# Kernel tuning notes

Measured on AMD Instinct MI355X. Metric: run time of the kernel, lower is better.

Reference implementation:

```python
import jax, jax.numpy as jnp
import numpy as np

NUM_HEADS = 8
OUT_FEATURES = 64
ALPHA = 0.2


def setup_inputs() -> dict:
    key = jax.random.key(0)
    k1, k2, k3, k4 = jax.random.split(key, 4)
    B, N, E, F_IN = 2, 8192, 4096, 256
    x = jax.random.normal(k1, (B, N, F_IN), dtype=jnp.float32)
    H = jax.random.uniform(k2, (N, E), dtype=jnp.float32)
    # xavier-like scaled params
    W = jax.random.normal(k3, (F_IN, OUT_FEATURES * NUM_HEADS), dtype=jnp.float32) * 0.05
    a_vertices = jax.random.normal(k4, (OUT_FEATURES, 1), dtype=jnp.float32) * 0.1
    return {"x": x, "H": H, "W": W, "a_vertices": a_vertices}


def reference(x, H, W, a_vertices):
    B, N, _ = x.shape
    # Wh: (B, N, heads, out)
    Wh = jnp.matmul(x, W).reshape(B, N, NUM_HEADS, OUT_FEATURES)
    # per-node, per-head attention logit: (B, N, heads)
    av = jax.nn.leaky_relu(jnp.einsum('bnhd,d->bnh', Wh, a_vertices[:, 0]), ALPHA)
    # edge attention: softmax over edges (torch dim=0 of (E, heads))
    ae = jax.nn.softmax(jnp.einsum('ne,bnh->beh', H, av), axis=1)  # (B, E, heads)
    # aggregate node features onto edges: (B, E, heads, out)
    m = jnp.einsum('ne,bnhd->behd', H, Wh)
    # scatter back to nodes with edge-attention weighting: (B, N, heads, out)
    out = jnp.einsum('ne,beh,behd->bnhd', H, ae, m)
    return out.reshape(B, N, NUM_HEADS * OUT_FEATURES)
```

## Files before the change

kernel.cpp:

```cpp
#include <hip/hip_runtime.h>

#define N_NODES 8192
#define N_EDGES 4096
#define F_INS   256
#define HEADS   8
#define DOUT    64
#define HDIM    512
#define CCOMB   1024
#define BATCH   2

typedef __bf16 bf16x8 __attribute__((ext_vector_type(8)));
typedef __bf16 bf16x4 __attribute__((ext_vector_type(4)));
typedef float  f32x4  __attribute__((ext_vector_type(4)));

__device__ __forceinline__ void gld_lds16(const __bf16* g, __bf16* l) {
    __builtin_amdgcn_global_load_lds(
        (const __attribute__((address_space(1))) void*)g,
        (__attribute__((address_space(3))) void*)l, 16, 0, 0);
}

__launch_bounds__(256)
__global__ void convert_H_logits_kernel(const float* __restrict__ H,
                                        const float* __restrict__ av,
                                        __bf16* __restrict__ Hb,
                                        __bf16* __restrict__ HbT,
                                        float* __restrict__ logits) {
    __shared__ float lav[512 * 16];
    __shared__ __bf16 tile[32][33];
    __shared__ float red[256 * 16];
    int t = threadIdx.x;
    int e0 = blockIdx.x * 32;
    int n0 = blockIdx.y * 512;
    for (int p = t; p < 8192; p += 256) {
        int b = p >> 12, rem = p & 4095, i = rem >> 3, h = rem & 7;
        lav[i * 16 + b * 8 + h] = av[(size_t)b * (N_NODES * 8) + (size_t)(n0 + i) * 8 + h];
    }
    __syncthreads();
    int c = t & 31, r0 = t >> 5;
    float acc[16];
#pragma unroll
    for (int q = 0; q < 16; ++q) acc[q] = 0.f;
    for (int sub = 0; sub < 16; ++sub) {
        int nb = n0 + sub * 32;
#pragma unroll
        for (int p = 0; p < 4; ++p) {
            int r = p * 8 + r0;
            float v = H[(size_t)(nb + r) * N_EDGES + e0 + c];
            __bf16 bv = (__bf16)v;
            Hb[(size_t)(nb + r) * N_EDGES + e0 + c] = bv;
            tile[r][c] = bv;
            const float* lr = &lav[(sub * 32 + r) * 16];
#pragma unroll
            for (int q = 0; q < 16; ++q) acc[q] += v * lr[q];
        }
        __syncthreads();
#pragma unroll
        for (int p = 0; p < 4; ++p) {
            int er = p * 8 + r0;
            HbT[(size_t)(e0 + er) * N_NODES + nb + c] = tile[c][er];
        }
        __syncthreads();
    }
#pragma unroll
    for (int q = 0; q < 16; ++q) red[t * 16 + q] = acc[q];
    __syncthreads();
    for (int o = t; o < 512; o += 256) {
        int e = o & 31, q = o >> 5;
        float s = 0.f;
#pragma unroll
        for (int r8 = 0; r8 < 8; ++r8) s += red[(r8 * 32 + e) * 16 + q];
        atomicAdd(&logits[(size_t)q * N_EDGES + e0 + e], s);
    }
}

__launch_bounds__(256)
__global__ void wbt_kernel(const float* __restrict__ W, __bf16* __restrict__ WbT) {
    int i = blockIdx.x * 256 + threadIdx.x;
    int c = i >> 8, f = i & 255;
    WbT[i] = (__bf16)W[(size_t)f * HDIM + c];
}

__launch_bounds__(256)
__global__ void wa_kernel(const float* __restrict__ W, const float* __restrict__ a,
                          float* __restrict__ Wa) {
    int i = blockIdx.x * 256 + threadIdx.x;
    if (i >= F_INS * HEADS) return;
    int f = i >> 3, h = i & 7;
    float s = 0.f;
#pragma unroll 8
    for (int d = 0; d < DOUT; ++d) s += W[(size_t)f * HDIM + h * DOUT + d] * a[d];
    Wa[i] = s;
}

__launch_bounds__(256)
__global__ void av_kernel(const float* __restrict__ x, const float* __restrict__ Wa,
                          float* __restrict__ av, __bf16* __restrict__ xb) {
    __shared__ float lx[32][257];
    __shared__ float lwa[F_INS * HEADS];
    int t = threadIdx.x;
    size_t row0 = (size_t)blockIdx.x * 32;
    for (int p = t; p < F_INS * HEADS; p += 256) lwa[p] = Wa[p];
#pragma unroll
    for (int p = 0; p < 32; ++p) {
        float v = x[(row0 + p) * F_INS + t];
        lx[p][t] = v;
        xb[(row0 + p) * F_INS + t] = (__bf16)v;
    }
    __syncthreads();
    int r = t >> 3, h = t & 7;
    float acc = 0.f;
#pragma unroll 8
    for (int f = 0; f < F_INS; ++f) acc += lx[r][f] * lwa[f * 8 + h];
    av[(row0 + r) * 8 + h] = acc > 0.f ? acc : 0.2f * acc;
}

__launch_bounds__(256)
__global__ void softmax_kernel(float* __restrict__ logits) {
    __shared__ float red[4];
    __shared__ float reds[4];
    int t = threadIdx.x;
    float* row = logits + (size_t)blockIdx.x * N_EDGES;
    float mx = -1e30f;
    for (int i = t; i < N_EDGES; i += 256) mx = fmaxf(mx, row[i]);
#pragma unroll
    for (int o = 32; o > 0; o >>= 1) mx = fmaxf(mx, __shfl_xor(mx, o, 64));
    if ((t & 63) == 0) red[t >> 6] = mx;
    __syncthreads();
    mx = fmaxf(fmaxf(red[0], red[1]), fmaxf(red[2], red[3]));
    float s = 0.f;
    for (int i = t; i < N_EDGES; i += 256) {
        float v = expf(row[i] - mx);
        row[i] = v;
        s += v;
    }
#pragma unroll
    for (int o = 32; o > 0; o >>= 1) s += __shfl_xor(s, o, 64);
    if ((t & 63) == 0) reds[t >> 6] = s;
    __syncthreads();
    float inv = 1.0f / (reds[0] + reds[1] + reds[2] + reds[3]);
    for (int i = t; i < N_EDGES; i += 256) row[i] *= inv;
}

template <int MODE>
__launch_bounds__(256, 3)
__global__ void gemm_bt(const __bf16* __restrict__ A, const __bf16* __restrict__ BT,
                        int lda, int ldbt, int K,
                        size_t a_bz, size_t bt_bz, size_t out_z,
                        __bf16* __restrict__ outB, int ldo,
                        float* __restrict__ outF) {
    __shared__ __bf16 AsF[8192];
    __shared__ __bf16 BsF[8192];
    int t = threadIdx.x;

    int bx, by, bz;
    if (MODE == 0) {
        bx = blockIdx.x; by = blockIdx.y; bz = blockIdx.z;
    } else if (MODE == 1) {
        int bid = blockIdx.x;
        int xcd = bid & 7, local = bid >> 3;
        bz = local >> 5;
        int rem = local & 31;
        bx = xcd * 4 + (rem >> 3);
        by = rem & 7;
    } else {
        int bid = blockIdx.x;
        bx = bid & 7; by = bid >> 3; bz = 0;
    }

    A  += (size_t)bz * a_bz;
    BT += (size_t)bz * bt_bz;
    if (MODE == 0) outB += (size_t)bz * out_z;
    if (MODE == 1) outF += (size_t)bz * out_z;
    size_t m0 = (size_t)by * 128;
    size_t n0 = (size_t)bx * 128;

    int lane = t & 63, wv = t >> 6;
    int ln = lane & 15, lk = lane >> 4;

    const __bf16* pA[4]; const __bf16* pB[4];
    __bf16* lA[4]; __bf16* lB[4];
#pragma unroll
    for (int p = 0; p < 4; ++p) {
        int bid = wv * 4 + p;
        int mb = bid >> 1, kb = bid & 1;
        pA[p] = A + (m0 + mb * 16 + ln) * (size_t)lda + kb * 32 + lk * 8;
        pB[p] = BT + (n0 + mb * 16 + ln) * (size_t)ldbt + kb * 32 + lk * 8;
        lA[p] = &AsF[bid * 512];
        lB[p] = &BsF[bid * 512];
    }

    int wm16 = (wv & 1) * 4, wn16 = (wv >> 1) * 4;
    f32x4 acc[4][4] = {};

    for (int k0 = 0; k0 < K; k0 += 64) {
        __syncthreads();
#pragma unroll
        for (int p = 0; p < 4; ++p) gld_lds16(pA[p] + k0, lA[p]);
#pragma unroll
        for (int p = 0; p < 4; ++p) gld_lds16(pB[p] + k0, lB[p]);
        __syncthreads();
        bf16x8 af[2][4], bfr[2][4];
#pragma unroll
        for (int ksb = 0; ksb < 2; ++ksb) {
#pragma unroll
            for (int i = 0; i < 4; ++i)
                af[ksb][i] = *(const bf16x8*)&AsF[((wm16 + i) * 2 + ksb) * 512 + lane * 8];
#pragma unroll
            for (int j = 0; j < 4; ++j)
                bfr[ksb][j] = *(const bf16x8*)&BsF[((wn16 + j) * 2 + ksb) * 512 + lane * 8];
        }
#pragma unroll
        for (int ksb = 0; ksb < 2; ++ksb)
#pragma unroll
            for (int i = 0; i < 4; ++i)
#pragma unroll
                for (int j = 0; j < 4; ++j)
                    acc[i][j] = __builtin_amdgcn_mfma_f32_16x16x32_bf16(
                        af[ksb][i], bfr[ksb][j], acc[i][j], 0, 0, 0);
    }

    int wm = (wv & 1) * 64, wn = (wv >> 1) * 64;
#pragma unroll
    for (int i = 0; i < 4; ++i)
#pragma unroll
        for (int j = 0; j < 4; ++j)
#pragma unroll
            for (int rg = 0; rg < 4; ++rg) {
                int gm = (int)m0 + wm + i * 16 + lk * 4 + rg;
                int gc = (int)n0 + wn + j * 16 + ln;
                float v = acc[i][j][rg];
                if (MODE == 0) {
                    outB[(size_t)gm * ldo + gc] = (__bf16)v;
                } else if (MODE == 1) {
                    outF[(size_t)gm * ldo + gc] = v;
                } else {
                    outF[(size_t)(gc >> 9) * ((size_t)N_NODES * HDIM) +
                         (size_t)gm * HDIM + (gc & 511)] = v;
                }
            }
}

__launch_bounds__(256)
__global__ void scale1_kernel(const float* __restrict__ acc1, const float* __restrict__ ae,
                              __bf16* __restrict__ mwT) {
    int i = blockIdx.x * 256 + threadIdx.x;
    size_t base = (size_t)i * 4;
    int c = (int)(base >> 12);
    int e = (int)(base & 4095);
    const size_t slab = (size_t)CCOMB * N_EDGES / 4;
    float4 s0 = ((const float4*)acc1)[i];
    float4 s1 = ((const float4*)acc1)[i + slab];
    float4 s2 = ((const float4*)acc1)[i + 2 * slab];
    float4 s3 = ((const float4*)acc1)[i + 3 * slab];
    float4 a4 = *(const float4*)(ae + ((size_t)(c >> 6) << 12) + e);
    bf16x4 o;
    o.x = (__bf16)((s0.x + s1.x + s2.x + s3.x) * a4.x);
    o.y = (__bf16)((s0.y + s1.y + s2.y + s3.y) * a4.y);
    o.z = (__bf16)((s0.z + s1.z + s2.z + s3.z) * a4.z);
    o.w = (__bf16)((s0.w + s1.w + s2.w + s3.w) * a4.w);
    ((bf16x4*)mwT)[i] = o;
}

extern "C" void kernel_launch(void* const* d_in, const int* in_sizes, int n_in,
                              void* d_out, int out_size, void* d_ws, size_t ws_size,
                              hipStream_t stream) {
    const float* x = (const float*)d_in[0];
    const float* H = (const float*)d_in[1];
    const float* W = (const float*)d_in[2];
    const float* a = (const float*)d_in[3];
    float* out = (float*)d_out;

    char* p = (char*)d_ws;
    __bf16* Hb   = (__bf16*)p; p += (size_t)N_NODES * N_EDGES * 2;
    __bf16* HbT  = (__bf16*)p; p += (size_t)N_EDGES * N_NODES * 2;
    __bf16* xb   = (__bf16*)p; p += (size_t)BATCH * N_NODES * F_INS * 2;
    __bf16* WbT  = (__bf16*)p; p += (size_t)HDIM * F_INS * 2;
    __bf16* WhbT = (__bf16*)p; p += (size_t)CCOMB * N_NODES * 2;
    __bf16* mwT  = (__bf16*)p; p += (size_t)CCOMB * N_EDGES * 2;
    float*  Wa   = (float*)p;  p += (size_t)F_INS * HEADS * 4;
    float*  av   = (float*)p;  p += (size_t)BATCH * N_NODES * HEADS * 4;
    float*  ae   = (float*)p;  p += (size_t)16 * N_EDGES * 4;
    float*  acc1 = (float*)p;  p += (size_t)4 * CCOMB * N_EDGES * 4;

    hipMemsetAsync(ae, 0, (size_t)16 * N_EDGES * 4, stream);

    wbt_kernel<<<dim3(HDIM * F_INS / 256), 256, 0, stream>>>(W, WbT);
    wa_kernel<<<dim3(8), 256, 0, stream>>>(W, a, Wa);
    av_kernel<<<dim3(BATCH * N_NODES / 32), 256, 0, stream>>>(x, Wa, av, xb);
    convert_H_logits_kernel<<<dim3(N_EDGES / 32, N_NODES / 512), 256, 0, stream>>>(
        H, av, Hb, HbT, ae);
    softmax_kernel<<<dim3(16), 256, 0, stream>>>(ae);

    gemm_bt<0><<<dim3(64, 4, 2), 256, 0, stream>>>(
        WbT, xb, F_INS, F_INS, F_INS,
        0, (size_t)N_NODES * F_INS, (size_t)HDIM * N_NODES,
        WhbT, N_NODES, nullptr);

    gemm_bt<1><<<dim3(1024), 256, 0, stream>>>(
        WhbT, HbT, N_NODES, N_NODES, 2048,
        2048, 2048, (size_t)CCOMB * N_EDGES,
        nullptr, N_EDGES, acc1);

    scale1_kernel<<<dim3(CCOMB * N_EDGES / 4 / 256), 256, 0, stream>>>(acc1, ae, mwT);

    gemm_bt<2><<<dim3(512), 256, 0, stream>>>(
        Hb, mwT, N_EDGES, N_EDGES, N_EDGES,
        0, 0, 0,
        nullptr, 0, out);
}
```

Before: 568.0 us.

## Triple-buffer GEMM LDS tiles with async prefetch two K-steps ahead

Replaces the single-buffered 64-wide K loop with a 3-stage ring of 32-wide K tiles in LDS. Global-to-LDS loads are issued two iterations ahead, with manual vmcnt waits and raw s_barrier. The goal is to hide global load latency behind the MFMA work instead of stalling at every step. In exchange the loop runs twice as many iterations with a smaller K step, and the hand-counted vmcnt waits and barriers risk races if the counts are wrong.

```diff
diff --git a/kernel.cpp b/kernel.cpp
--- a/kernel.cpp
+++ b/kernel.cpp
@@ -148,8 +148,8 @@
                         size_t a_bz, size_t bt_bz, size_t out_z,
                         __bf16* __restrict__ outB, int ldo,
                         float* __restrict__ outF) {
-    __shared__ __bf16 AsF[8192];
-    __shared__ __bf16 BsF[8192];
+    __shared__ __bf16 AsF[3][4096];
+    __shared__ __bf16 BsF[3][4096];
     int t = threadIdx.x;
 
     int bx, by, bz;
@@ -177,46 +177,65 @@
     int lane = t & 63, wv = t >> 6;
     int ln = lane & 15, lk = lane >> 4;
 
-    const __bf16* pA[4]; const __bf16* pB[4];
-    __bf16* lA[4]; __bf16* lB[4];
-#pragma unroll
-    for (int p = 0; p < 4; ++p) {
-        int bid = wv * 4 + p;
-        int mb = bid >> 1, kb = bid & 1;
-        pA[p] = A + (m0 + mb * 16 + ln) * (size_t)lda + kb * 32 + lk * 8;
-        pB[p] = BT + (n0 + mb * 16 + ln) * (size_t)ldbt + kb * 32 + lk * 8;
-        lA[p] = &AsF[bid * 512];
-        lB[p] = &BsF[bid * 512];
-    }
+    const __bf16* gA[2]; const __bf16* gB[2];
+#pragma unroll
+    for (int p = 0; p < 2; ++p) {
+        int mb = wv * 2 + p;
+        gA[p] = A + (m0 + mb * 16 + ln) * (size_t)lda + lk * 8;
+        gB[p] = BT + (n0 + mb * 16 + ln) * (size_t)ldbt + lk * 8;
+    }
+    __bf16* lA = &AsF[0][(wv * 2) * 512];
+    __bf16* lB = &BsF[0][(wv * 2) * 512];
 
     int wm16 = (wv & 1) * 4, wn16 = (wv >> 1) * 4;
     f32x4 acc[4][4] = {};
 
-    for (int k0 = 0; k0 < K; k0 += 64) {
-        __syncthreads();
-#pragma unroll
-        for (int p = 0; p < 4; ++p) gld_lds16(pA[p] + k0, lA[p]);
-#pragma unroll
-        for (int p = 0; p < 4; ++p) gld_lds16(pB[p] + k0, lB[p]);
-        __syncthreads();
-        bf16x8 af[2][4], bfr[2][4];
-#pragma unroll
-        for (int ksb = 0; ksb < 2; ++ksb) {
-#pragma unroll
-            for (int i = 0; i < 4; ++i)
-                af[ksb][i] = *(const bf16x8*)&AsF[((wm16 + i) * 2 + ksb) * 512 + lane * 8];
+    const int iters = K >> 5;
+
+    {
+        gld_lds16(gA[0], lA);
+        gld_lds16(gA[1], lA + 512);
+        gld_lds16(gB[0], lB);
+        gld_lds16(gB[1], lB + 512);
+        gld_lds16(gA[0] + 32, lA + 4096);
+        gld_lds16(gA[1] + 32, lA + 4096 + 512);
+        gld_lds16(gB[0] + 32, lB + 4096);
+        gld_lds16(gB[1] + 32, lB + 4096 + 512);
+    }
+
+    int cur = 0;
+    for (int it = 0; it < iters; ++it) {
+        if (it + 2 < iters) {
+            int st = cur + 2; if (st >= 3) st -= 3;
+            int ko = (it + 2) << 5;
+            gld_lds16(gA[0] + ko, lA + st * 4096);
+            gld_lds16(gA[1] + ko, lA + st * 4096 + 512);
+            gld_lds16(gB[0] + ko, lB + st * 4096);
+            gld_lds16(gB[1] + ko, lB + st * 4096 + 512);
+            asm volatile("s_waitcnt vmcnt(8)" ::: "memory");
+        } else if (it + 1 < iters) {
+            asm volatile("s_waitcnt vmcnt(4)" ::: "memory");
+        } else {
+            asm volatile("s_waitcnt vmcnt(0)" ::: "memory");
+        }
+        asm volatile("s_barrier" ::: "memory");
+
+        bf16x8 af[4], bfr[4];
+#pragma unroll
+        for (int i = 0; i < 4; ++i)
+            af[i] = *(const bf16x8*)&AsF[cur][(wm16 + i) * 512 + lane * 8];
+#pragma unroll
+        for (int j = 0; j < 4; ++j)
+            bfr[j] = *(const bf16x8*)&BsF[cur][(wn16 + j) * 512 + lane * 8];
+#pragma unroll
+        for (int i = 0; i < 4; ++i)
 #pragma unroll
             for (int j = 0; j < 4; ++j)
-                bfr[ksb][j] = *(const bf16x8*)&BsF[((wn16 + j) * 2 + ksb) * 512 + lane * 8];
-        }
-#pragma unroll
-        for (int ksb = 0; ksb < 2; ++ksb)
-#pragma unroll
-            for (int i = 0; i < 4; ++i)
-#pragma unroll
-                for (int j = 0; j < 4; ++j)
-                    acc[i][j] = __builtin_amdgcn_mfma_f32_16x16x32_bf16(
-                        af[ksb][i], bfr[ksb][j], acc[i][j], 0, 0, 0);
+                acc[i][j] = __builtin_amdgcn_mfma_f32_16x16x32_bf16(
+                    af[i], bfr[j], acc[i][j], 0, 0, 0);
+
+        asm volatile("s_barrier" ::: "memory");
+        cur = cur + 1; if (cur == 3) cur = 0;
     }
 
     int wm = (wv & 1) * 64, wn = (wv >> 1) * 64;
```

Result: slower. 606.5 us (+6.8%).
